# Kernel optimization log

Measured on AMD Instinct MI355X. Metric: run time of the kernel, lower is better.

Reference implementation:

```python
import jax, jax.numpy as jnp
import numpy as np

NEG_SLOPE = 0.2


def gat_conv(h, src, dst, n_dst, W_src, W_dst, attn_l, attn_r, bias):
    # h: [N_src, F_in]; edges src->dst; dst nodes are a prefix of src nodes.
    H, D = attn_l.shape
    z_src = (h @ W_src).reshape(h.shape[0], H, D)          # [N_src, H, D]
    z_dst = (h[:n_dst] @ W_dst).reshape(n_dst, H, D)       # [N_dst, H, D]
    el = jnp.einsum('nhd,hd->nh', z_src, attn_l)           # [N_src, H]
    er = jnp.einsum('nhd,hd->nh', z_dst, attn_r)           # [N_dst, H]
    e = jax.nn.leaky_relu(el[src] + er[dst], NEG_SLOPE)    # [E, H]
    # numerically stable edge softmax over incoming edges of each dst node
    m = jax.ops.segment_max(e, dst, num_segments=n_dst)    # [N_dst, H]
    w = jnp.exp(e - m[dst])                                # [E, H]
    s = jax.ops.segment_sum(w, dst, num_segments=n_dst)    # [N_dst, H]
    alpha = w / s[dst]                                     # [E, H]
    msg = alpha[:, :, None] * z_src[src]                   # [E, H, D]
    out = jax.ops.segment_sum(msg, dst, num_segments=n_dst)
    return out + bias                                      # [N_dst, H, D]


def setup_inputs() -> dict:
    key = jax.random.key(0)
    ks = jax.random.split(key, 16)
    IN, HID, HEADS, NCLS = 256, 64, 4, 47
    N_SRC0, N_DST0, E0 = 200000, 50000, 500000
    N_DST1, E1 = 10000, 100000
    sc0 = 0.1
    inp = {
        'x': jax.random.normal(ks[0], (N_SRC0, IN), jnp.float32),
        'src0': jax.random.randint(ks[1], (E0,), 0, N_SRC0, jnp.int32),
        'dst0': jax.random.randint(ks[2], (E0,), 0, N_DST0, jnp.int32),
        'src1': jax.random.randint(ks[3], (E1,), 0, N_DST0, jnp.int32),
        'dst1': jax.random.randint(ks[4], (E1,), 0, N_DST1, jnp.int32),
        'num_dst0': N_DST0,
        'num_dst1': N_DST1,
        'W0_src': jax.random.normal(ks[5], (IN, HEADS * HID), jnp.float32) * sc0,
        'W0_dst': jax.random.normal(ks[6], (IN, HEADS * HID), jnp.float32) * sc0,
        'attn_l0': jax.random.normal(ks[7], (HEADS, HID), jnp.float32) * sc0,
        'attn_r0': jax.random.normal(ks[8], (HEADS, HID), jnp.float32) * sc0,
        'bias0': jnp.zeros((HEADS, HID), jnp.float32),
        'W1_src': jax.random.normal(ks[9], (HEADS * HID, HEADS * NCLS), jnp.float32) * sc0,
        'W1_dst': jax.random.normal(ks[10], (HEADS * HID, HEADS * NCLS), jnp.float32) * sc0,
        'attn_l1': jax.random.normal(ks[11], (HEADS, NCLS), jnp.float32) * sc0,
        'attn_r1': jax.random.normal(ks[12], (HEADS, NCLS), jnp.float32) * sc0,
        'bias1': jnp.zeros((HEADS, NCLS), jnp.float32),
    }
    return inp


def reference(x, src0, dst0, src1, dst1, num_dst0, num_dst1,
              W0_src, W0_dst, attn_l0, attn_r0, bias0,
              W1_src, W1_dst, attn_l1, attn_r1, bias1):
    # layer 0: GATConv + relu activation, flatten heads
    h = gat_conv(x, src0, dst0, num_dst0, W0_src, W0_dst, attn_l0, attn_r0, bias0)
    h = jax.nn.relu(h).reshape(num_dst0, -1)               # [N_dst0, H*HID]
    # layer 1: GATConv, no activation
    h = gat_conv(h, src1, dst1, num_dst1, W1_src, W1_dst, attn_l1, attn_r1, bias1)
    h = h.mean(axis=1)                                     # mean over heads -> [N_dst1, n_classes]
    return jax.nn.log_softmax(h, axis=-1)
```

## Files before the change

### kernel.cpp

```cpp
#include <hip/hip_runtime.h>
#include <math.h>

typedef _Float16 half8 __attribute__((ext_vector_type(8)));
typedef _Float16 half4 __attribute__((ext_vector_type(4)));
typedef float f32x16 __attribute__((ext_vector_type(16)));

constexpr int IN    = 256;
constexpr int NCLS  = 47;
constexpr int HD1   = 188;
constexpr float NEG_SLOPE = 0.2f;
constexpr int ND0 = 50000, ND1 = 10000;

static __device__ __forceinline__ float leaky(float x) {
    return x >= 0.f ? x : NEG_SLOPE * x;
}

__device__ __forceinline__ void gload16(const void* g, void* l) {
    __builtin_amdgcn_global_load_lds((const __attribute__((address_space(1))) void*)g,
                                     (__attribute__((address_space(3))) void*)l, 16, 0, 0);
}

__global__ __launch_bounds__(256) void prep_k(
        const float* __restrict__ W0s, const float* __restrict__ W1s,
        const float* __restrict__ W0d, const float* __restrict__ W1d,
        const float* __restrict__ al0, const float* __restrict__ ar0,
        const float* __restrict__ al1, const float* __restrict__ ar1,
        _Float16* __restrict__ B0t, _Float16* __restrict__ B1t,
        float* __restrict__ vl0T, float* __restrict__ vr0T,
        float* __restrict__ vl1T, float* __restrict__ vr1T) {
    int b = blockIdx.x, t = threadIdx.x;
    if (b < 256) {
        int id = b * 256 + t;
        int n = id >> 8, k = id & 255;
        B0t[n * 256 + k] = (_Float16)W0s[(size_t)k * 256 + n];
    } else if (b < 448) {
        int id = (b - 256) * 256 + t;
        int n = id >> 8, k = id & 255;
        B1t[n * 256 + k] = (n < HD1) ? (_Float16)W1s[(size_t)k * HD1 + n] : (_Float16)0.f;
    } else if (b == 448) {
        for (int i = t; i < 1024; i += 256) {
            int h = i >> 8, k = i & 255;
            float s = 0.f;
            for (int d = 0; d < 64; ++d)
                s += W0d[(size_t)k * 256 + h * 64 + d] * ar0[h * 64 + d];
            vr0T[h * 256 + k] = s;
        }
    } else if (b == 449) {
        for (int i = t; i < 1024; i += 256) {
            int h = i >> 8, k = i & 255;
            float s = 0.f;
            for (int d = 0; d < 64; ++d)
                s += W0s[(size_t)k * 256 + h * 64 + d] * al0[h * 64 + d];
            vl0T[h * 256 + k] = s;
        }
    } else if (b == 450) {
        for (int i = t; i < 1024; i += 256) {
            int h = i >> 8, k = i & 255;
            float s = 0.f;
            for (int d = 0; d < NCLS; ++d)
                s += W1s[(size_t)k * HD1 + h * NCLS + d] * al1[h * NCLS + d];
            vl1T[h * 256 + k] = s;
        }
    } else {
        for (int i = t; i < 1024; i += 256) {
            int h = i >> 8, k = i & 255;
            float s = 0.f;
            for (int d = 0; d < NCLS; ++d)
                s += W1d[(size_t)k * HD1 + h * NCLS + d] * ar1[h * NCLS + d];
            vr1T[h * 256 + k] = s;
        }
    }
}

__global__ __launch_bounds__(256) void cvt_lr(const float* __restrict__ x,
        const float* __restrict__ vlT, const float* __restrict__ vrT,
        _Float16* __restrict__ xh, float* __restrict__ el, float* __restrict__ er,
        int M, int Mr) {
    int wv = threadIdx.x >> 6, lane = threadIdx.x & 63;
    int row = blockIdx.x * 4 + wv;
    if (row >= M) return;
    float4 xa = *(const float4*)(x + (size_t)row * IN + lane * 4);
    half4 hv;
    hv[0] = (_Float16)xa.x; hv[1] = (_Float16)xa.y;
    hv[2] = (_Float16)xa.z; hv[3] = (_Float16)xa.w;
    *(half4*)(xh + (size_t)row * IN + lane * 4) = hv;
    float sl[4], sr[4];
    bool do_r = row < Mr;
#pragma unroll
    for (int h = 0; h < 4; ++h) {
        float4 v = *(const float4*)(vlT + h * IN + lane * 4);
        sl[h] = xa.x * v.x + xa.y * v.y + xa.z * v.z + xa.w * v.w;
        float4 u = *(const float4*)(vrT + h * IN + lane * 4);
        sr[h] = xa.x * u.x + xa.y * u.y + xa.z * u.z + xa.w * u.w;
    }
#pragma unroll
    for (int off = 32; off; off >>= 1)
#pragma unroll
        for (int h = 0; h < 4; ++h) {
            sl[h] += __shfl_xor(sl[h], off);
            sr[h] += __shfl_xor(sr[h], off);
        }
    if (lane == 0) {
        *(float4*)(el + (size_t)row * 4) = make_float4(sl[0], sl[1], sl[2], sl[3]);
        if (do_r)
            *(float4*)(er + (size_t)row * 4) = make_float4(sr[0], sr[1], sr[2], sr[3]);
    }
}

template <int NWC>
__global__ __launch_bounds__(512, 4) void gemmd(const _Float16* __restrict__ Ah,
        const _Float16* __restrict__ Bt, _Float16* __restrict__ Z, int M, int ntiles) {
    __shared__ __align__(16) char As[4][16384];
    const int t = threadIdx.x, l = t & 63, w = t >> 6;
    const int l31 = l & 31, hi = l >> 5;
    const int G = gridDim.x;
    const int tile0 = blockIdx.x;

    half8 wk[16];
    {
        int wc = (w < NWC) ? w * 32 + l31 : 0;
        const _Float16* bp = Bt + (size_t)wc * 256 + hi * 8;
#pragma unroll
        for (int ks = 0; ks < 16; ++ks) wk[ks] = *(const half8*)(bp + ks * 16);
    }

    auto stage = [&](int it) {
        int tile = tile0 + it * G;
        if (tile >= ntiles) return;
        char* dst = As[it & 3];
#pragma unroll
        for (int i = 0; i < 2; ++i) {
            int c = i * 512 + t;
            int r = c >> 5, s = c & 31;
            int row = tile * 32 + r; if (row >= M) row = M - 1;
            gload16(Ah + (size_t)row * 256 + ((s ^ r) << 3), dst + c * 16);
        }
    };

    int nit = 0;
    if (tile0 < ntiles) nit = (ntiles - 1 - tile0) / G + 1;

    stage(0); stage(1); stage(2);
    for (int it = 0; it < nit; ++it) {
        asm volatile("s_waitcnt vmcnt(4)" ::: "memory");
        __syncthreads();
        stage(it + 3);
        if (w < NWC) {
            const char* buf = As[it & 3];
            f32x16 acc;
#pragma unroll
            for (int e = 0; e < 16; ++e) acc[e] = 0.f;
#pragma unroll
            for (int ks = 0; ks < 16; ++ks) {
                half8 bf = *(const half8*)(buf + l31 * 512 + (((2 * ks + hi) ^ l31) << 4));
                acc = __builtin_amdgcn_mfma_f32_32x32x16_f16(wk[ks], bf, acc, 0, 0, 0);
            }
            int xrow = (tile0 + it * G) * 32 + l31;
            if (xrow < M) {
#pragma unroll
                for (int g = 0; g < 4; ++g) {
                    half4 hv;
                    hv[0] = (_Float16)acc[g * 4 + 0]; hv[1] = (_Float16)acc[g * 4 + 1];
                    hv[2] = (_Float16)acc[g * 4 + 2]; hv[3] = (_Float16)acc[g * 4 + 3];
                    *(half4*)(Z + (size_t)xrow * (NWC * 32) + w * 32 + g * 8 + hi * 4) = hv;
                }
            }
        }
    }
}

__global__ __launch_bounds__(256) void gemv_lr_f16(const _Float16* __restrict__ A,
        const float* __restrict__ vlT, const float* __restrict__ vrT,
        float* __restrict__ el, float* __restrict__ er, int M, int Mr) {
    int wv = threadIdx.x >> 6, lane = threadIdx.x & 63;
    int row = blockIdx.x * 4 + wv;
    if (row >= M) return;
    half4 ah = *(const half4*)(A + (size_t)row * IN + lane * 4);
    float a0 = (float)ah[0], a1 = (float)ah[1], a2 = (float)ah[2], a3 = (float)ah[3];
    float sl[4], sr[4];
#pragma unroll
    for (int h = 0; h < 4; ++h) {
        float4 v = *(const float4*)(vlT + h * IN + lane * 4);
        sl[h] = a0 * v.x + a1 * v.y + a2 * v.z + a3 * v.w;
        float4 u = *(const float4*)(vrT + h * IN + lane * 4);
        sr[h] = a0 * u.x + a1 * u.y + a2 * u.z + a3 * u.w;
    }
#pragma unroll
    for (int off = 32; off; off >>= 1)
#pragma unroll
        for (int h = 0; h < 4; ++h) {
            sl[h] += __shfl_xor(sl[h], off);
            sr[h] += __shfl_xor(sr[h], off);
        }
    if (lane == 0) {
        *(float4*)(el + (size_t)row * 4) = make_float4(sl[0], sl[1], sl[2], sl[3]);
        if (row < Mr)
            *(float4*)(er + (size_t)row * 4) = make_float4(sr[0], sr[1], sr[2], sr[3]);
    }
}

__global__ void hist2_k(const int* __restrict__ dst0, int E0,
                        const int* __restrict__ dst1, int E1, int* __restrict__ counts) {
    int i = blockIdx.x * blockDim.x + threadIdx.x;
    if (i < E0) atomicAdd(&counts[dst0[i]], 1);
    else if (i < E0 + E1) atomicAdd(&counts[ND0 + dst1[i - E0]], 1);
}

__global__ __launch_bounds__(256) void scan1_k(const int* __restrict__ counts, int n,
                                               int* __restrict__ part) {
    __shared__ int ws[4];
    int i = blockIdx.x * 256 + threadIdx.x;
    int lane = threadIdx.x & 63, wv = threadIdx.x >> 6;
    int s = (i < n) ? counts[i] : 0;
#pragma unroll
    for (int off = 32; off; off >>= 1) s += __shfl_xor(s, off);
    if (lane == 0) ws[wv] = s;
    __syncthreads();
    if (threadIdx.x == 0) part[blockIdx.x] = ws[0] + ws[1] + ws[2] + ws[3];
}

__global__ __launch_bounds__(256) void scan2_k(int* __restrict__ part, int nb) {
    __shared__ int ws[4];
    int tid = threadIdx.x, lane = tid & 63, wv = tid >> 6;
    int v = (tid < nb) ? part[tid] : 0;
    int x = v;
#pragma unroll
    for (int off = 1; off < 64; off <<= 1) {
        int u = __shfl_up(x, off);
        if (lane >= off) x += u;
    }
    if (lane == 63) ws[wv] = x;
    __syncthreads();
    int base = 0;
    for (int k = 0; k < wv; ++k) base += ws[k];
    if (tid < nb) part[tid] = base + x - v;
}

__global__ __launch_bounds__(256) void scan3_k(const int* __restrict__ counts, int n,
        const int* __restrict__ part, int* __restrict__ offsets, int* __restrict__ cursor) {
    __shared__ int ws[4];
    int i = blockIdx.x * 256 + threadIdx.x;
    int lane = threadIdx.x & 63, wv = threadIdx.x >> 6;
    int v = (i < n) ? counts[i] : 0;
    int x = v;
#pragma unroll
    for (int off = 1; off < 64; off <<= 1) {
        int u = __shfl_up(x, off);
        if (lane >= off) x += u;
    }
    if (lane == 63) ws[wv] = x;
    __syncthreads();
    int base = part[blockIdx.x];
    for (int k = 0; k < wv; ++k) base += ws[k];
    int off_ = base + x - v;
    if (i < n) { offsets[i] = off_; cursor[i] = off_; }
    if (i == n - 1) offsets[n] = off_ + v;
}

__global__ void scatter2_k(const int* __restrict__ src0, const int* __restrict__ dst0, int E0,
                           const int* __restrict__ src1, const int* __restrict__ dst1, int E1,
                           int* __restrict__ cursor, int* __restrict__ ssrc) {
    int i = blockIdx.x * blockDim.x + threadIdx.x;
    if (i < E0) {
        int p = atomicAdd(&cursor[dst0[i]], 1);
        ssrc[p] = src0[i];
    } else if (i < E0 + E1) {
        int j = i - E0;
        int p = atomicAdd(&cursor[ND0 + dst1[j]], 1);
        ssrc[p] = src1[j];
    }
}

__global__ __launch_bounds__(256) void agg_l0(const int* __restrict__ ssrc,
        const int* __restrict__ offs, const float* __restrict__ el,
        const float* __restrict__ er, const _Float16* __restrict__ z,
        const float* __restrict__ bias, _Float16* __restrict__ h, int nd) {
    int wv = threadIdx.x >> 6, lane = threadIdx.x & 63;
    int d = blockIdx.x * 4 + wv;
    if (d >= nd) return;
    int head = lane >> 4;
    int beg = offs[d], end = offs[d + 1];
    float erh = er[(size_t)d * 4 + head];
    float ax = 0, ay = 0, az = 0, aw = 0, ssum = 0;
    for (int j0 = beg; j0 < end; j0 += 64) {
        int nn = min(64, end - j0);
        int myidx = (lane < nn) ? ssrc[j0 + lane] : 0;
        int j = 0;
        for (; j + 4 <= nn; j += 4) {
            int s0 = __shfl(myidx, j),     s1 = __shfl(myidx, j + 1);
            int s2 = __shfl(myidx, j + 2), s3 = __shfl(myidx, j + 3);
            float e0 = el[(size_t)s0 * 4 + head], e1 = el[(size_t)s1 * 4 + head];
            float e2 = el[(size_t)s2 * 4 + head], e3 = el[(size_t)s3 * 4 + head];
            half4 zv0 = *(const half4*)(z + (size_t)s0 * 256 + lane * 4);
            half4 zv1 = *(const half4*)(z + (size_t)s1 * 256 + lane * 4);
            half4 zv2 = *(const half4*)(z + (size_t)s2 * 256 + lane * 4);
            half4 zv3 = *(const half4*)(z + (size_t)s3 * 256 + lane * 4);
            float w0 = __expf(leaky(e0 + erh)), w1 = __expf(leaky(e1 + erh));
            float w2 = __expf(leaky(e2 + erh)), w3 = __expf(leaky(e3 + erh));
            ssum += (w0 + w1) + (w2 + w3);
            ax += w0 * (float)zv0[0] + w1 * (float)zv1[0] + w2 * (float)zv2[0] + w3 * (float)zv3[0];
            ay += w0 * (float)zv0[1] + w1 * (float)zv1[1] + w2 * (float)zv2[1] + w3 * (float)zv3[1];
            az += w0 * (float)zv0[2] + w1 * (float)zv1[2] + w2 * (float)zv2[2] + w3 * (float)zv3[2];
            aw += w0 * (float)zv0[3] + w1 * (float)zv1[3] + w2 * (float)zv2[3] + w3 * (float)zv3[3];
        }
        for (; j < nn; ++j) {
            int s = __shfl(myidx, j);
            float e = el[(size_t)s * 4 + head] + erh;
            float wgt = __expf(leaky(e));
            ssum += wgt;
            half4 zv = *(const half4*)(z + (size_t)s * 256 + lane * 4);
            ax += wgt * (float)zv[0]; ay += wgt * (float)zv[1];
            az += wgt * (float)zv[2]; aw += wgt * (float)zv[3];
        }
    }
    float inv = ssum > 0.f ? 1.f / ssum : 0.f;
    const float* b = bias + lane * 4;
    half4 o;
    o[0] = (_Float16)fmaxf(ax * inv + b[0], 0.f);
    o[1] = (_Float16)fmaxf(ay * inv + b[1], 0.f);
    o[2] = (_Float16)fmaxf(az * inv + b[2], 0.f);
    o[3] = (_Float16)fmaxf(aw * inv + b[3], 0.f);
    *(half4*)(h + (size_t)d * 256 + lane * 4) = o;
}

__global__ __launch_bounds__(256) void agg_l1f(const int* __restrict__ ssrc,
        const int* __restrict__ offs, const float* __restrict__ el,
        const float* __restrict__ er, const _Float16* __restrict__ z,
        const float* __restrict__ bias, float* __restrict__ y, int nd) {
    __shared__ float ro[4][192];
    int wv = threadIdx.x >> 6, lane = threadIdx.x & 63;
    int d = blockIdx.x * 4 + wv;
    if (d >= nd) return;
    int beg = offs[ND0 + d], end = offs[ND0 + d + 1];
    float4 er4 = *(const float4*)(er + (size_t)d * 4);
    const int f0 = lane, f1 = lane + 64, f2 = lane + 128;
    const int h0 = f0 / NCLS, h1 = f1 / NCLS;
    const bool has2 = f2 < HD1;
    const int h2 = has2 ? f2 / NCLS : 3;
    float a0 = 0, a1 = 0, a2 = 0;
    float s0 = 0, s1 = 0, s2 = 0, s3 = 0;
    for (int j0 = beg; j0 < end; j0 += 64) {
        int nn = min(64, end - j0);
        int myidx = (lane < nn) ? ssrc[j0 + lane] : 0;
        int j = 0;
        for (; j + 2 <= nn; j += 2) {
            int sa_ = __shfl(myidx, j), sb_ = __shfl(myidx, j + 1);
            float4 ea = *(const float4*)(el + (size_t)sa_ * 4);
            float4 eb = *(const float4*)(el + (size_t)sb_ * 4);
            const _Float16* za = z + (size_t)sa_ * 192;
            const _Float16* zb = z + (size_t)sb_ * 192;
            float za0 = (float)za[f0], za1 = (float)za[f1], za2 = has2 ? (float)za[f2] : 0.f;
            float zb0 = (float)zb[f0], zb1 = (float)zb[f1], zb2 = has2 ? (float)zb[f2] : 0.f;
            float wa0 = __expf(leaky(ea.x + er4.x)), wa1 = __expf(leaky(ea.y + er4.y));
            float wa2 = __expf(leaky(ea.z + er4.z)), wa3 = __expf(leaky(ea.w + er4.w));
            float wb0 = __expf(leaky(eb.x + er4.x)), wb1 = __expf(leaky(eb.y + er4.y));
            float wb2 = __expf(leaky(eb.z + er4.z)), wb3 = __expf(leaky(eb.w + er4.w));
            s0 += wa0 + wb0; s1 += wa1 + wb1; s2 += wa2 + wb2; s3 += wa3 + wb3;
            a0 += (h0 == 0 ? wa0 : h0 == 1 ? wa1 : h0 == 2 ? wa2 : wa3) * za0
                + (h0 == 0 ? wb0 : h0 == 1 ? wb1 : h0 == 2 ? wb2 : wb3) * zb0;
            a1 += (h1 == 0 ? wa0 : h1 == 1 ? wa1 : h1 == 2 ? wa2 : wa3) * za1
                + (h1 == 0 ? wb0 : h1 == 1 ? wb1 : h1 == 2 ? wb2 : wb3) * zb1;
            if (has2)
                a2 += (h2 == 0 ? wa0 : h2 == 1 ? wa1 : h2 == 2 ? wa2 : wa3) * za2
                    + (h2 == 0 ? wb0 : h2 == 1 ? wb1 : h2 == 2 ? wb2 : wb3) * zb2;
        }
        for (; j < nn; ++j) {
            int s = __shfl(myidx, j);
            float4 e4 = *(const float4*)(el + (size_t)s * 4);
            float w0 = __expf(leaky(e4.x + er4.x));
            float w1 = __expf(leaky(e4.y + er4.y));
            float w2 = __expf(leaky(e4.z + er4.z));
            float w3 = __expf(leaky(e4.w + er4.w));
            s0 += w0; s1 += w1; s2 += w2; s3 += w3;
            const _Float16* zr = z + (size_t)s * 192;
            a0 += (h0 == 0 ? w0 : h0 == 1 ? w1 : h0 == 2 ? w2 : w3) * (float)zr[f0];
            a1 += (h1 == 0 ? w0 : h1 == 1 ? w1 : h1 == 2 ? w2 : w3) * (float)zr[f1];
            if (has2) a2 += (h2 == 0 ? w0 : h2 == 1 ? w1 : h2 == 2 ? w2 : w3) * (float)zr[f2];
        }
    }
    float sa = h0 == 0 ? s0 : h0 == 1 ? s1 : h0 == 2 ? s2 : s3;
    float sb = h1 == 0 ? s0 : h1 == 1 ? s1 : h1 == 2 ? s2 : s3;
    float sc = h2 == 0 ? s0 : h2 == 1 ? s1 : h2 == 2 ? s2 : s3;
    ro[wv][f0] = a0 * (sa > 0.f ? 1.f / sa : 0.f) + bias[f0];
    ro[wv][f1] = a1 * (sb > 0.f ? 1.f / sb : 0.f) + bias[f1];
    if (has2) ro[wv][f2] = a2 * (sc > 0.f ? 1.f / sc : 0.f) + bias[f2];
    asm volatile("s_waitcnt lgkmcnt(0)" ::: "memory");
    __builtin_amdgcn_sched_barrier(0);
    float vv = 0.f, v = -INFINITY;
    if (lane < NCLS) {
        vv = 0.25f * (ro[wv][lane] + ro[wv][lane + NCLS] +
                      ro[wv][lane + 2 * NCLS] + ro[wv][lane + 3 * NCLS]);
        v = vv;
    }
    float mx = v;
#pragma unroll
    for (int off = 32; off; off >>= 1) mx = fmaxf(mx, __shfl_xor(mx, off));
    float pp = (lane < NCLS) ? __expf(vv - mx) : 0.f;
    float sum = pp;
#pragma unroll
    for (int off = 32; off; off >>= 1) sum += __shfl_xor(sum, off);
    if (lane < NCLS) y[(size_t)d * NCLS + lane] = vv - mx - logf(sum);
}

extern "C" void kernel_launch(void* const* d_in, const int* in_sizes, int n_in,
                              void* d_out, int out_size, void* d_ws, size_t ws_size,
                              hipStream_t stream) {
    const float* x    = (const float*)d_in[0];
    const int*   src0 = (const int*)d_in[1];
    const int*   dst0 = (const int*)d_in[2];
    const int*   src1 = (const int*)d_in[3];
    const int*   dst1 = (const int*)d_in[4];
    const float* W0s  = (const float*)d_in[7];
    const float* W0d  = (const float*)d_in[8];
    const float* al0  = (const float*)d_in[9];
    const float* ar0  = (const float*)d_in[10];
    const float* b0   = (const float*)d_in[11];
    const float* W1s  = (const float*)d_in[12];
    const float* W1d  = (const float*)d_in[13];
    const float* al1  = (const float*)d_in[14];
    const float* ar1  = (const float*)d_in[15];
    const float* b1   = (const float*)d_in[16];
    const int E0 = in_sizes[1], E1 = in_sizes[3];
    const int NS0 = in_sizes[0] / IN;

    char* p = (char*)d_ws;
    auto take = [&](size_t bytes) {
        char* r = p;
        p += (bytes + 255) & ~(size_t)255;
        return r;
    };
    _Float16* xh   = (_Float16*)take((size_t)NS0 * 256 * 2);
    _Float16* z0   = (_Float16*)take((size_t)NS0 * 256 * 2);
    _Float16* h    = (_Float16*)take((size_t)ND0 * 256 * 2);
    _Float16* z1   = (_Float16*)take((size_t)ND0 * 192 * 2);
    float*    el0  = (float*)take((size_t)NS0 * 4 * 4);
    float*    er0  = (float*)take((size_t)ND0 * 4 * 4);
    float*    el1  = (float*)take((size_t)ND0 * 4 * 4);
    float*    er1  = (float*)take((size_t)ND1 * 4 * 4);
    _Float16* B0t  = (_Float16*)take((size_t)256 * 256 * 2);
    _Float16* B1t  = (_Float16*)take((size_t)192 * 256 * 2);
    float*    vl0T = (float*)take(4 * 256 * 4);
    float*    vr0T = (float*)take(4 * 256 * 4);
    float*    vl1T = (float*)take(4 * 256 * 4);
    float*    vr1T = (float*)take(4 * 256 * 4);
    const int NDT = ND0 + ND1;
    int* counts = (int*)take((size_t)NDT * 4);
    int* offs   = (int*)take((size_t)(NDT + 1) * 4);
    int* cur    = (int*)take((size_t)NDT * 4);
    int* ss     = (int*)take((size_t)(E0 + E1) * 4);
    int* part   = (int*)take(256 * 4);

    const int NB = (NDT + 255) / 256;
    const int NT0 = (NS0 + 31) / 32, NT1 = (ND0 + 31) / 32;
    const int G0 = NT0 < 512 ? NT0 : 512, G1 = NT1 < 512 ? NT1 : 512;

    hipMemsetAsync(counts, 0, (size_t)NDT * 4, stream);

    prep_k<<<452, 256, 0, stream>>>(W0s, W1s, W0d, W1d, al0, ar0, al1, ar1,
                                    B0t, B1t, vl0T, vr0T, vl1T, vr1T);
    hist2_k<<<(E0 + E1 + 255) / 256, 256, 0, stream>>>(dst0, E0, dst1, E1, counts);
    scan1_k<<<NB, 256, 0, stream>>>(counts, NDT, part);
    scan2_k<<<1, 256, 0, stream>>>(part, NB);
    scan3_k<<<NB, 256, 0, stream>>>(counts, NDT, part, offs, cur);
    scatter2_k<<<(E0 + E1 + 255) / 256, 256, 0, stream>>>(src0, dst0, E0, src1, dst1, E1,
                                                          cur, ss);

    cvt_lr<<<(NS0 + 3) / 4, 256, 0, stream>>>(x, vl0T, vr0T, xh, el0, er0, NS0, ND0);
    gemmd<8><<<G0, 512, 0, stream>>>(xh, B0t, z0, NS0, NT0);
    agg_l0<<<(ND0 + 3) / 4, 256, 0, stream>>>(ss, offs, el0, er0, z0, b0, h, ND0);

    gemmd<6><<<G1, 512, 0, stream>>>(h, B1t, z1, ND0, NT1);
    gemv_lr_f16<<<(ND0 + 3) / 4, 256, 0, stream>>>(h, vl1T, vr1T, el1, er1, ND0, ND1);
    agg_l1f<<<(ND1 + 3) / 4, 256, 0, stream>>>(ss, offs, el1, er1, z1, b1,
                                               (float*)d_out, ND1);
}
```

Measured before the change: 363.2 us.

## Restructure projection GEMM to keep full weight in LDS and stream A via registers

Replaces the GEMM that held a 32-column weight slice in registers and staged A tiles through LDS with a kernel that loads the whole swizzled weight matrix into LDS once per block. Each wave then streams 16-row A tiles directly into registers with double buffering and runs 16x16x32 MFMAs across all output columns. The weight transpose in prep is XOR-swizzled to avoid LDS bank conflicts. This aims to cut LDS staging and syncthreads per tile and make all waves do useful work. In exchange, output stores become scalar fp16 writes, and the 128 KB LDS footprint for 256 columns limits occupancy.

```diff
diff --git a/kernel.cpp b/kernel.cpp
--- a/kernel.cpp
+++ b/kernel.cpp
@@ -3,7 +3,7 @@
 
 typedef _Float16 half8 __attribute__((ext_vector_type(8)));
 typedef _Float16 half4 __attribute__((ext_vector_type(4)));
-typedef float f32x16 __attribute__((ext_vector_type(16)));
+typedef float f32x4 __attribute__((ext_vector_type(4)));
 
 constexpr int IN    = 256;
 constexpr int NCLS  = 47;
@@ -32,11 +32,13 @@
     if (b < 256) {
         int id = b * 256 + t;
         int n = id >> 8, k = id & 255;
-        B0t[n * 256 + k] = (_Float16)W0s[(size_t)k * 256 + n];
+        int dst = n * 256 + ((((k >> 3) ^ (n & 31)) & 31) << 3) + (k & 7);
+        B0t[dst] = (_Float16)W0s[(size_t)k * 256 + n];
     } else if (b < 448) {
         int id = (b - 256) * 256 + t;
         int n = id >> 8, k = id & 255;
-        B1t[n * 256 + k] = (n < HD1) ? (_Float16)W1s[(size_t)k * HD1 + n] : (_Float16)0.f;
+        int dst = n * 256 + ((((k >> 3) ^ (n & 31)) & 31) << 3) + (k & 7);
+        B1t[dst] = (n < HD1) ? (_Float16)W1s[(size_t)k * HD1 + n] : (_Float16)0.f;
     } else if (b == 448) {
         for (int i = t; i < 1024; i += 256) {
             int h = i >> 8, k = i & 255;
@@ -107,64 +109,80 @@
     }
 }
 
-template <int NWC>
-__global__ __launch_bounds__(512, 4) void gemmd(const _Float16* __restrict__ Ah,
-        const _Float16* __restrict__ Bt, _Float16* __restrict__ Z, int M, int ntiles) {
-    __shared__ __align__(16) char As[4][16384];
+template <int NCOLS>
+__global__ __launch_bounds__(512, 2) void gemmw(const _Float16* __restrict__ Ah,
+        const _Float16* __restrict__ BtS, _Float16* __restrict__ Z, int M, int ntiles) {
+    constexpr int NCF = NCOLS / 16;
+    __shared__ __align__(16) _Float16 Bs[NCOLS * 256];
     const int t = threadIdx.x, l = t & 63, w = t >> 6;
-    const int l31 = l & 31, hi = l >> 5;
-    const int G = gridDim.x;
-    const int tile0 = blockIdx.x;
-
-    half8 wk[16];
-    {
-        int wc = (w < NWC) ? w * 32 + l31 : 0;
-        const _Float16* bp = Bt + (size_t)wc * 256 + hi * 8;
-#pragma unroll
-        for (int ks = 0; ks < 16; ++ks) wk[ks] = *(const half8*)(bp + ks * 16);
-    }
-
-    auto stage = [&](int it) {
-        int tile = tile0 + it * G;
-        if (tile >= ntiles) return;
-        char* dst = As[it & 3];
-#pragma unroll
-        for (int i = 0; i < 2; ++i) {
-            int c = i * 512 + t;
-            int r = c >> 5, s = c & 31;
-            int row = tile * 32 + r; if (row >= M) row = M - 1;
-            gload16(Ah + (size_t)row * 256 + ((s ^ r) << 3), dst + c * 16);
-        }
+    const int lr = l & 15, lh = l >> 4;
+    constexpr int BI = (NCOLS * 256 * 2) / (512 * 16);
+#pragma unroll
+    for (int it = 0; it < BI; ++it) {
+        int c = it * 512 + t;
+        gload16(BtS + c * 8, (char*)Bs + c * 16);
+    }
+    __syncthreads();
+
+    const int NW = gridDim.x * 8;
+    const int gw = blockIdx.x * 8 + w;
+
+    half8 p0[8], p1[8];
+
+    auto issue = [&](int tile, half8 (&p)[8]) {
+        int row = tile * 16 + lr; if (row >= M) row = M - 1;
+        const _Float16* ap = Ah + (size_t)row * 256 + lh * 8;
+#pragma unroll
+        for (int ks = 0; ks < 8; ++ks) p[ks] = *(const half8*)(ap + ks * 32);
+        __builtin_amdgcn_sched_barrier(0);
     };
 
-    int nit = 0;
-    if (tile0 < ntiles) nit = (ntiles - 1 - tile0) / G + 1;
-
-    stage(0); stage(1); stage(2);
-    for (int it = 0; it < nit; ++it) {
-        asm volatile("s_waitcnt vmcnt(4)" ::: "memory");
-        __syncthreads();
-        stage(it + 3);
-        if (w < NWC) {
-            const char* buf = As[it & 3];
-            f32x16 acc;
-#pragma unroll
-            for (int e = 0; e < 16; ++e) acc[e] = 0.f;
-#pragma unroll
-            for (int ks = 0; ks < 16; ++ks) {
-                half8 bf = *(const half8*)(buf + l31 * 512 + (((2 * ks + hi) ^ l31) << 4));
-                acc = __builtin_amdgcn_mfma_f32_32x32x16_f16(wk[ks], bf, acc, 0, 0, 0);
+    auto compute = [&](int tile, half8 (&p)[8]) {
+        f32x4 acc[NCF];
+#pragma unroll
+        for (int cf = 0; cf < NCF; ++cf) {
+            acc[cf][0] = 0.f; acc[cf][1] = 0.f; acc[cf][2] = 0.f; acc[cf][3] = 0.f;
+        }
+#pragma unroll
+        for (int ks = 0; ks < 8; ++ks) {
+#pragma unroll
+            for (int cf = 0; cf < NCF; ++cf) {
+                int colr = cf * 16 + lr;
+                half8 bf = *(const half8*)&Bs[colr * 256 +
+                                              ((((ks * 4 + lh) ^ (colr & 31)) & 31) << 3)];
+                acc[cf] = __builtin_amdgcn_mfma_f32_16x16x32_f16(p[ks], bf, acc[cf], 0, 0, 0);
             }
-            int xrow = (tile0 + it * G) * 32 + l31;
+        }
+#pragma unroll
+        for (int r = 0; r < 4; ++r) {
+            int xrow = tile * 16 + lh * 4 + r;
             if (xrow < M) {
 #pragma unroll
-                for (int g = 0; g < 4; ++g) {
-                    half4 hv;
-                    hv[0] = (_Float16)acc[g * 4 + 0]; hv[1] = (_Float16)acc[g * 4 + 1];
-                    hv[2] = (_Float16)acc[g * 4 + 2]; hv[3] = (_Float16)acc[g * 4 + 3];
-                    *(half4*)(Z + (size_t)xrow * (NWC * 32) + w * 32 + g * 8 + hi * 4) = hv;
-                }
+                for (int cf = 0; cf < NCF; ++cf)
+                    Z[(size_t)xrow * NCOLS + cf * 16 + lr] = (_Float16)acc[cf][r];
             }
+        }
+    };
+
+    if (gw < ntiles) issue(gw, p0);
+    for (int tt = gw; tt < ntiles; tt += 2 * NW) {
+        int t1 = tt + NW;
+        if (t1 < ntiles) {
+            issue(t1, p1);
+            asm volatile("s_waitcnt vmcnt(8)" ::: "memory");
+        } else {
+            asm volatile("s_waitcnt vmcnt(0)" ::: "memory");
+        }
+        compute(tt, p0);
+        if (t1 < ntiles) {
+            int t2 = tt + 2 * NW;
+            if (t2 < ntiles) {
+                issue(t2, p0);
+                asm volatile("s_waitcnt vmcnt(8)" ::: "memory");
+            } else {
+                asm volatile("s_waitcnt vmcnt(0)" ::: "memory");
+            }
+            compute(t1, p1);
         }
     }
 }
@@ -451,8 +469,7 @@
     int* part   = (int*)take(256 * 4);
 
     const int NB = (NDT + 255) / 256;
-    const int NT0 = (NS0 + 31) / 32, NT1 = (ND0 + 31) / 32;
-    const int G0 = NT0 < 512 ? NT0 : 512, G1 = NT1 < 512 ? NT1 : 512;
+    const int NT0 = (NS0 + 15) / 16, NT1 = (ND0 + 15) / 16;
 
     hipMemsetAsync(counts, 0, (size_t)NDT * 4, stream);
 
@@ -466,10 +483,10 @@
                                                           cur, ss);
 
     cvt_lr<<<(NS0 + 3) / 4, 256, 0, stream>>>(x, vl0T, vr0T, xh, el0, er0, NS0, ND0);
-    gemmd<8><<<G0, 512, 0, stream>>>(xh, B0t, z0, NS0, NT0);
+    gemmw<256><<<256, 512, 0, stream>>>(xh, B0t, z0, NS0, NT0);
     agg_l0<<<(ND0 + 3) / 4, 256, 0, stream>>>(ss, offs, el0, er0, z0, b0, h, ND0);
 
-    gemmd<6><<<G1, 512, 0, stream>>>(h, B1t, z1, ND0, NT1);
+    gemmw<192><<<256, 512, 0, stream>>>(h, B1t, z1, ND0, NT1);
     gemv_lr_f16<<<(ND0 + 3) / 4, 256, 0, stream>>>(h, vl1T, vr1T, el1, er1, ND0, ND1);
     agg_l1f<<<(ND1 + 3) / 4, 256, 0, stream>>>(ss, offs, el1, er1, z1, b1,
                                                (float*)d_out, ND1);
```

New measurement: 358.5 us. No clear change (-1.3%).
